# Performance work log

Measured on AMD Instinct MI355X. Metric: run time of the kernel, lower is better.

Reference implementation:

```python
import jax, jax.numpy as jnp
import numpy as np

SYNCNET_T = 5
EMB_D = 512


def _l2norm(x, eps=1e-12):
    return x / jnp.maximum(jnp.linalg.norm(x, axis=-1, keepdims=True), eps)


def setup_inputs() -> dict:
    key = jax.random.key(0)
    k = jax.random.split(key, 6)
    b = 256
    a_1 = jax.random.normal(k[0], (b, 1, 80, 16), dtype=jnp.float32)
    a_2 = jax.random.normal(k[1], (b, 1, 80, 16), dtype=jnp.float32)
    v_1 = jax.random.normal(k[2], (b, 3, SYNCNET_T, 96, 96), dtype=jnp.float32)
    v_2 = jax.random.normal(k[3], (b, 3, SYNCNET_T, 96, 96), dtype=jnp.float32)
    da = 1 * 80 * 16
    dv = 3 * SYNCNET_T * 48 * 96
    W_a = jax.random.normal(k[4], (da, EMB_D), dtype=jnp.float32) / np.float32(np.sqrt(da))
    W_v = jax.random.normal(k[5], (dv, EMB_D), dtype=jnp.float32) / np.float32(np.sqrt(dv))
    return {"a_1": a_1, "v_1": v_1, "a_2": a_2, "v_2": v_2, "W_a": W_a, "W_v": W_v}


def reference(a_1, v_1, a_2, v_2, W_a, W_v):
    b = a_1.shape[0]
    audio = jnp.concatenate([a_1, a_2], axis=0)      # (2b,1,80,16)
    visual = jnp.concatenate([v_1, v_2], axis=0)     # (2b,3,T,96,96)
    visual = visual[:, :, :, visual.shape[3] // 2:]  # lower half -> (2b,3,T,48,96)
    # torch.cat([visual[:,:,i] for i in range(T)], dim=1) -> channel order (T,3)
    n2 = visual.shape[0]
    visual = jnp.moveaxis(visual, 2, 1).reshape(n2, 3 * SYNCNET_T, 48, 96)
    # syncnet (modeled): flatten -> linear -> L2 normalize, 512-d embeddings
    a = _l2norm(audio.reshape(n2, -1) @ W_a)  # (2b,d)
    v = _l2norm(visual.reshape(n2, -1) @ W_v)  # (2b,d)
    a1, a2 = a[:b], a[b:]
    v1, v2 = v[:b], v[b:]
    dot = lambda x, y: jnp.sum(x * y, axis=-1)
    # numerator: product of {a1,a2}x{v1,v2} + combos within audio and within visual
    numerator = (jnp.exp(dot(a1, v1)) + jnp.exp(dot(a1, v2))
                 + jnp.exp(dot(a2, v1)) + jnp.exp(dot(a2, v2))
                 + jnp.exp(dot(a1, a2)) + jnp.exp(dot(v1, v2)))  # (b,)
    # denominator: product of {a1,a2} with ALL visual embeddings v (2b)
    denominator = (jnp.exp(a1 @ v.T) + jnp.exp(a2 @ v.T)).sum(axis=1)  # (b,)
    loss = -jnp.mean(jnp.log(numerator / denominator))
    return loss
```

## Files before the change

### kernel.cpp

```cpp
#include <hip/hip_runtime.h>

typedef __attribute__((ext_vector_type(8))) short bf16x8;
typedef __attribute__((ext_vector_type(4))) float f32x4;

#define KSPLIT_V 16
#define KSPLIT_A 4

__device__ __forceinline__ unsigned int pk2(float a, float b) {
    unsigned int r;
    asm("v_cvt_pk_bf16_f32 %0, %1, %2" : "=v"(r) : "v"(a), "v"(b));
    return r;
}

template<int MODE>
__global__ __launch_bounds__(256, 4) void mm_kernel(
    const float* __restrict__ s1, const float* __restrict__ s2,
    const float* __restrict__ Bsrc, float* __restrict__ outp,
    float* __restrict__ den, float* __restrict__ num)
{
    __shared__ uint4 As[2][256];
    __shared__ uint4 Bs[2][256];

    const int tid = threadIdx.x;
    const int blk = blockIdx.x;

    int m0, n0, k0, nsteps, z = 0;
    if (MODE == 0) {
        const int lin = (blk & 7) * 128 + (blk >> 3);
        z  = lin >> 6;
        m0 = ((lin >> 3) & 7) * 64;
        n0 = (lin & 7) * 64;
        k0 = z * 4320;
        nsteps = 135;
    } else if (MODE == 1) {
        z  = blk >> 6;
        m0 = ((blk >> 3) & 7) * 64;
        n0 = (blk & 7) * 64;
        k0 = z * 320;
        nsteps = 10;
    } else {
        m0 = (blk >> 3) * 64;
        n0 = (blk & 7) * 64;
        k0 = 0;
        nsteps = 16;
    }
    if (MODE != 2) outp += (size_t)z * (512 * 512);

    const int ROWSTR = (MODE == 0) ? 138240 : (MODE == 1 ? 1280 : 512);

    const int a_row = tid >> 2;
    const int a_kb  = tid & 3;
    const int b_col = tid & 63;
    const int b_kb  = tid >> 6;
    const int a_u = (a_kb * 64 + a_row) ^ (a_kb << 1);
    const int b_u = (b_kb * 64 + b_col) ^ (b_kb << 1);

    const int grow = m0 + a_row;
    const float* abase = (grow < 256) ? (s1 + (size_t)grow * ROWSTR)
                                      : (s2 + (size_t)(grow - 256) * ROWSTR);
    int aoff, jj = 0, kglob = k0;
    if (MODE == 0) {
        const int ph = k0 / 4608;
        jj = k0 - ph * 4608;
        const int c = ph % 3, t = ph / 3;
        aoff = c * 46080 + t * 9216 + 4608 + jj + a_kb * 8;
    } else {
        aoff = k0 + a_kb * 8;
    }

    const float* bptr;
    if (MODE == 2) bptr = Bsrc + (size_t)(n0 + b_col) * 512 + b_kb * 8;
    else           bptr = Bsrc + (size_t)(k0 + b_kb * 8) * 512 + n0 + b_col;

    const int lane = tid & 63;
    const int wid  = tid >> 6;
    const int wrow = (wid >> 1) * 32;
    const int wcol = (wid & 1) * 32;
    const int l15  = lane & 15;
    const int lk   = lane >> 4;

    int ra[2], rb[2];
    #pragma unroll
    for (int m = 0; m < 2; ++m) ra[m] = (lk * 64 + wrow + m * 16 + l15) ^ (lk << 1);
    #pragma unroll
    for (int n = 0; n < 2; ++n) rb[n] = (lk * 64 + wcol + n * 16 + l15) ^ (lk << 1);

    f32x4 acc[2][2];
    #pragma unroll
    for (int m = 0; m < 2; ++m)
        #pragma unroll
        for (int n = 0; n < 2; ++n) acc[m][n] = f32x4{0.f, 0.f, 0.f, 0.f};

    float4 A0 = *(const float4*)(abase + aoff);
    float4 A1 = *(const float4*)(abase + aoff + 4);
    float4 B0, B1; float bsr[8];
    if (MODE == 2) {
        B0 = *(const float4*)bptr; B1 = *(const float4*)(bptr + 4);
    } else {
        #pragma unroll
        for (int j = 0; j < 8; ++j) bsr[j] = bptr[(size_t)j * 512];
    }

    for (int ks = 0; ks < nsteps; ++ks) {
        const int cur = ks & 1;

        const bool more = (ks + 1 < nsteps);
        float4 A0n, A1n, B0n, B1n; float bsn[8];
        if (more) {
            kglob += 32;
            if (MODE == 0) {
                aoff += 32; jj += 32;
                if (jj == 4608) {
                    jj = 0;
                    const int ph = kglob / 4608;
                    const int c = ph % 3, t = ph / 3;
                    aoff = c * 46080 + t * 9216 + 4608 + a_kb * 8;
                }
            } else {
                aoff += 32;
            }
            A0n = *(const float4*)(abase + aoff);
            A1n = *(const float4*)(abase + aoff + 4);
            if (MODE == 2) {
                bptr += 32;
                B0n = *(const float4*)bptr; B1n = *(const float4*)(bptr + 4);
            } else {
                bptr += 32 * 512;
                #pragma unroll
                for (int j = 0; j < 8; ++j) bsn[j] = bptr[(size_t)j * 512];
            }
        }

        uint4 pa;
        pa.x = pk2(A0.x, A0.y); pa.y = pk2(A0.z, A0.w);
        pa.z = pk2(A1.x, A1.y); pa.w = pk2(A1.z, A1.w);
        As[cur][a_u] = pa;
        uint4 pb;
        if (MODE == 2) {
            pb.x = pk2(B0.x, B0.y); pb.y = pk2(B0.z, B0.w);
            pb.z = pk2(B1.x, B1.y); pb.w = pk2(B1.z, B1.w);
        } else {
            pb.x = pk2(bsr[0], bsr[1]); pb.y = pk2(bsr[2], bsr[3]);
            pb.z = pk2(bsr[4], bsr[5]); pb.w = pk2(bsr[6], bsr[7]);
        }
        Bs[cur][b_u] = pb;
        __syncthreads();

        bf16x8 af[2], bfr[2];
        #pragma unroll
        for (int m = 0; m < 2; ++m) af[m] = __builtin_bit_cast(bf16x8, As[cur][ra[m]]);
        #pragma unroll
        for (int n = 0; n < 2; ++n) bfr[n] = __builtin_bit_cast(bf16x8, Bs[cur][rb[n]]);
        #pragma unroll
        for (int m = 0; m < 2; ++m)
            #pragma unroll
            for (int n = 0; n < 2; ++n)
                acc[m][n] = __builtin_amdgcn_mfma_f32_16x16x32_bf16(af[m], bfr[n], acc[m][n], 0, 0, 0);

        if (more) {
            A0 = A0n; A1 = A1n;
            if (MODE == 2) { B0 = B0n; B1 = B1n; }
            else {
                #pragma unroll
                for (int j = 0; j < 8; ++j) bsr[j] = bsn[j];
            }
        }
    }

    if (MODE != 2) {
        #pragma unroll
        for (int m = 0; m < 2; ++m)
            #pragma unroll
            for (int n = 0; n < 2; ++n) {
                const int col = n0 + wcol + n * 16 + l15;
                #pragma unroll
                for (int r = 0; r < 4; ++r) {
                    const int row = m0 + wrow + m * 16 + lk * 4 + r;
                    outp[(size_t)row * 512 + col] = acc[m][n][r];
                }
            }
    } else {
        #pragma unroll
        for (int m = 0; m < 2; ++m) {
            float rs[4] = {0.f, 0.f, 0.f, 0.f};
            #pragma unroll
            for (int n = 0; n < 2; ++n) {
                const int col = n0 + wcol + n * 16 + l15;
                #pragma unroll
                for (int r = 0; r < 4; ++r) {
                    const int row = m0 + wrow + m * 16 + lk * 4 + r;
                    const float e = __expf(acc[m][n][r]);
                    rs[r] += e;
                    if (((row - col) & 255) == 0) atomicAdd(num + (row & 255), e);
                }
            }
            #pragma unroll
            for (int r = 0; r < 4; ++r) {
                float v = rs[r];
                v += __shfl_xor(v, 1);
                v += __shfl_xor(v, 2);
                v += __shfl_xor(v, 4);
                v += __shfl_xor(v, 8);
                if (l15 == 0) {
                    const int row = m0 + wrow + m * 16 + lk * 4 + r;
                    atomicAdd(den + (row & 255), v);
                }
            }
        }
    }
}

__global__ __launch_bounds__(256) void norm_kernel(
    const float* __restrict__ partA, const float* __restrict__ partV,
    float* __restrict__ Aout, float* __restrict__ Vout)
{
    const int row = blockIdx.x;
    const int tid = threadIdx.x;
    const bool isV = row >= 512;
    const int r = isV ? (row - 512) : row;
    const int c0 = tid, c1 = tid + 256;

    float v0 = 0.f, v1 = 0.f;
    if (isV) {
        #pragma unroll
        for (int zz = 0; zz < KSPLIT_V; ++zz) {
            const float* p = partV + (size_t)zz * 262144 + (size_t)r * 512;
            v0 += p[c0]; v1 += p[c1];
        }
    } else {
        #pragma unroll
        for (int zz = 0; zz < KSPLIT_A; ++zz) {
            const float* p = partA + (size_t)zz * 262144 + (size_t)r * 512;
            v0 += p[c0]; v1 += p[c1];
        }
    }

    float ss = v0 * v0 + v1 * v1;
    #pragma unroll
    for (int off = 32; off > 0; off >>= 1) ss += __shfl_down(ss, off);
    __shared__ float sbuf[4];
    if ((tid & 63) == 0) sbuf[tid >> 6] = ss;
    __syncthreads();
    const float total = sbuf[0] + sbuf[1] + sbuf[2] + sbuf[3];
    const float inv = 1.f / fmaxf(sqrtf(total), 1e-12f);

    float* outp = (isV ? Vout : Aout) + (size_t)r * 512;
    outp[c0] = v0 * inv;
    outp[c1] = v1 * inv;
}

__global__ __launch_bounds__(512) void zero_kernel(float* __restrict__ p) {
    p[threadIdx.x] = 0.f;
}

__global__ __launch_bounds__(256) void dots_kernel(
    const float* __restrict__ A, const float* __restrict__ V,
    float* __restrict__ num)
{
    const int b = blockIdx.x;
    const int i = b & 255;
    const float* X = (b < 256) ? A : V;
    const float* x = X + (size_t)i * 512;
    const float* y = X + (size_t)(i + 256) * 512;
    const int tid = threadIdx.x;
    float d = x[tid] * y[tid] + x[tid + 256] * y[tid + 256];
    #pragma unroll
    for (int off = 32; off > 0; off >>= 1) d += __shfl_down(d, off);
    __shared__ float sbuf[4];
    if ((tid & 63) == 0) sbuf[tid >> 6] = d;
    __syncthreads();
    if (tid == 0) atomicAdd(num + i, __expf(sbuf[0] + sbuf[1] + sbuf[2] + sbuf[3]));
}

__global__ __launch_bounds__(256) void final_kernel(
    const float* __restrict__ den, const float* __restrict__ num,
    float* __restrict__ out)
{
    const int tid = threadIdx.x;
    float v = logf(den[tid]) - logf(num[tid]);
    #pragma unroll
    for (int off = 32; off > 0; off >>= 1) v += __shfl_down(v, off);
    __shared__ float sbuf[4];
    if ((tid & 63) == 0) sbuf[tid >> 6] = v;
    __syncthreads();
    if (tid == 0) out[0] = (sbuf[0] + sbuf[1] + sbuf[2] + sbuf[3]) * (1.f / 256.f);
}

extern "C" void kernel_launch(void* const* d_in, const int* in_sizes, int n_in,
                              void* d_out, int out_size, void* d_ws, size_t ws_size,
                              hipStream_t stream)
{
    (void)in_sizes; (void)n_in; (void)out_size; (void)ws_size;
    const float* a_1 = (const float*)d_in[0];
    const float* v_1 = (const float*)d_in[1];
    const float* a_2 = (const float*)d_in[2];
    const float* v_2 = (const float*)d_in[3];
    const float* W_a = (const float*)d_in[4];
    const float* W_v = (const float*)d_in[5];
    float* out = (float*)d_out;

    float* ws      = (float*)d_ws;
    float* partV   = ws;
    float* partA   = partV + (size_t)KSPLIT_V * 262144;
    float* Anorm   = partA + (size_t)KSPLIT_A * 262144;
    float* Vnorm   = Anorm + 262144;
    float* den     = Vnorm + 262144;
    float* num     = den + 256;

    zero_kernel<<<1, 512, 0, stream>>>(den);
    mm_kernel<0><<<1024, 256, 0, stream>>>(v_1, v_2, W_v, partV, nullptr, nullptr);
    mm_kernel<1><<<256, 256, 0, stream>>>(a_1, a_2, W_a, partA, nullptr, nullptr);
    norm_kernel<<<1024, 256, 0, stream>>>(partA, partV, Anorm, Vnorm);
    mm_kernel<2><<<64, 256, 0, stream>>>(Anorm, Anorm + 256 * 512, Vnorm, nullptr, den, num);
    dots_kernel<<<512, 256, 0, stream>>>(Anorm, Vnorm, num);
    final_kernel<<<1, 256, 0, stream>>>(den, num, out);
}
```

Measured before the change: 176.0 us.

## Pre-convert inputs and weights to bf16 transposed, use 128x128 direct-to-LDS GEMM

Adds a fused pre-pass that converts W_v and W_a to transposed bf16 and, if the workspace is large enough, also converts the visual and audio activations to contiguous bf16. The main GEMM becomes a 128x128-tile kernel that fills LDS with global_load_lds, with a split-K count chosen from the workspace size. The similarity GEMM moves into its own kernel. The aim is to halve GEMM operand traffic and replace the strided scalar weight loads with wide loads, at the cost of an extra full conversion pass over the 70MB weight every call.

Result: slower. 199.8 us (+13.5%).

```diff
diff --git a/kernel.cpp b/kernel.cpp
--- a/kernel.cpp
+++ b/kernel.cpp
@@ -2,9 +2,6 @@
 
 typedef __attribute__((ext_vector_type(8))) short bf16x8;
 typedef __attribute__((ext_vector_type(4))) float f32x4;
-
-#define KSPLIT_V 16
-#define KSPLIT_A 4
 
 __device__ __forceinline__ unsigned int pk2(float a, float b) {
     unsigned int r;
@@ -12,207 +9,214 @@
     return r;
 }
 
-template<int MODE>
-__global__ __launch_bounds__(256, 4) void mm_kernel(
+__device__ __forceinline__ void gll16(void* lds, const void* g) {
+    __builtin_amdgcn_global_load_lds(
+        (__attribute__((address_space(1))) void*)(uintptr_t)g,
+        (__attribute__((address_space(3))) void*)(uint32_t)(uintptr_t)lds,
+        16, 0, 0);
+}
+
+__global__ __launch_bounds__(256) void conv_fused(
+    const float* __restrict__ v_1, const float* __restrict__ v_2,
+    const float* __restrict__ a_1, const float* __restrict__ a_2,
+    const float* __restrict__ W_v, const float* __restrict__ W_a,
+    unsigned short* __restrict__ Av, unsigned short* __restrict__ Wt,
+    unsigned short* __restrict__ Aa, unsigned short* __restrict__ Wat,
+    int doAv)
+{
+    __shared__ float T[64][65];
+    const int tid = threadIdx.x;
+    const int b = blockIdx.x;
+
+    if (b < 8800) {
+        const float* src; unsigned short* dst; int K, kt, nt;
+        if (b < 8640) { src = W_v; dst = Wt;  K = 69120; kt = b >> 3; nt = b & 7; }
+        else          { src = W_a; dst = Wat; K = 1280;  kt = (b - 8640) >> 3; nt = (b - 8640) & 7; }
+        const int k0 = kt * 64, n0 = nt * 64;
+        #pragma unroll
+        for (int i = 0; i < 4; ++i) {
+            const int kr = i * 16 + (tid >> 4);
+            const int c4 = tid & 15;
+            const float4 f = *(const float4*)(src + (size_t)(k0 + kr) * 512 + n0 + c4 * 4);
+            T[c4 * 4 + 0][kr] = f.x; T[c4 * 4 + 1][kr] = f.y;
+            T[c4 * 4 + 2][kr] = f.z; T[c4 * 4 + 3][kr] = f.w;
+        }
+        __syncthreads();
+        #pragma unroll
+        for (int j = 0; j < 2; ++j) {
+            const int id = j * 256 + tid;
+            const int nl = id >> 3, u = id & 7;
+            float v[8];
+            #pragma unroll
+            for (int kk = 0; kk < 8; ++kk) v[kk] = T[nl][u * 8 + kk];
+            uint4 o;
+            o.x = pk2(v[0], v[1]); o.y = pk2(v[2], v[3]);
+            o.z = pk2(v[4], v[5]); o.w = pk2(v[6], v[7]);
+            *(uint4*)(dst + (size_t)(n0 + nl) * K + k0 + u * 8) = o;
+        }
+    } else if (b < 16480) {
+        if (!doAv) return;
+        const int bb = b - 8800;
+        const int r = bb / 15, p = bb - r * 15;
+        const float* srcb = (r < 256) ? (v_1 + (size_t)r * 138240)
+                                      : (v_2 + (size_t)(r - 256) * 138240);
+        const int c = p % 3, t9 = p / 3;
+        const float* src = srcb + c * 46080 + t9 * 9216 + 4608;
+        unsigned short* dst = Av + (size_t)r * 69120 + p * 4608;
+        #pragma unroll
+        for (int it = 0; it < 5; ++it) {
+            const int u = it * 256 + tid;
+            if (u < 1152) {
+                const float4 f = *(const float4*)(src + u * 4);
+                uint2 o; o.x = pk2(f.x, f.y); o.y = pk2(f.z, f.w);
+                *(uint2*)(dst + u * 4) = o;
+            }
+        }
+    } else {
+        const int idx4 = (b - 16480) * 256 + tid;
+        const int row = idx4 / 320;
+        const int col4 = idx4 - row * 320;
+        const float* src = (row < 256) ? (a_1 + (size_t)row * 1280)
+                                       : (a_2 + (size_t)(row - 256) * 1280);
+        const float4 f = *(const float4*)(src + col4 * 4);
+        uint2 o; o.x = pk2(f.x, f.y); o.y = pk2(f.z, f.w);
+        *(uint2*)(Aa + (size_t)idx4 * 4) = o;
+    }
+}
+
+template<int AMODE>
+__global__ __launch_bounds__(256, 3) void gemm_kernel(
+    const unsigned short* __restrict__ Abf,
     const float* __restrict__ s1, const float* __restrict__ s2,
-    const float* __restrict__ Bsrc, float* __restrict__ outp,
-    float* __restrict__ den, float* __restrict__ num)
-{
-    __shared__ uint4 As[2][256];
-    __shared__ uint4 Bs[2][256];
+    const unsigned short* __restrict__ Bt,
+    float* __restrict__ part, int K, int ksteps)
+{
+    __shared__ uint4 As[1024];
+    __shared__ uint4 Bs[1024];
 
     const int tid = threadIdx.x;
     const int blk = blockIdx.x;
-
-    int m0, n0, k0, nsteps, z = 0;
-    if (MODE == 0) {
-        const int lin = (blk & 7) * 128 + (blk >> 3);
-        z  = lin >> 6;
-        m0 = ((lin >> 3) & 7) * 64;
-        n0 = (lin & 7) * 64;
-        k0 = z * 4320;
-        nsteps = 135;
-    } else if (MODE == 1) {
-        z  = blk >> 6;
-        m0 = ((blk >> 3) & 7) * 64;
-        n0 = (blk & 7) * 64;
-        k0 = z * 320;
-        nsteps = 10;
-    } else {
-        m0 = (blk >> 3) * 64;
-        n0 = (blk & 7) * 64;
-        k0 = 0;
-        nsteps = 16;
-    }
-    if (MODE != 2) outp += (size_t)z * (512 * 512);
-
-    const int ROWSTR = (MODE == 0) ? 138240 : (MODE == 1 ? 1280 : 512);
-
-    const int a_row = tid >> 2;
-    const int a_kb  = tid & 3;
-    const int b_col = tid & 63;
-    const int b_kb  = tid >> 6;
-    const int a_u = (a_kb * 64 + a_row) ^ (a_kb << 1);
-    const int b_u = (b_kb * 64 + b_col) ^ (b_kb << 1);
-
-    const int grow = m0 + a_row;
-    const float* abase = (grow < 256) ? (s1 + (size_t)grow * ROWSTR)
-                                      : (s2 + (size_t)(grow - 256) * ROWSTR);
-    int aoff, jj = 0, kglob = k0;
-    if (MODE == 0) {
-        const int ph = k0 / 4608;
-        jj = k0 - ph * 4608;
-        const int c = ph % 3, t = ph / 3;
-        aoff = c * 46080 + t * 9216 + 4608 + jj + a_kb * 8;
-    } else {
-        aoff = k0 + a_kb * 8;
-    }
-
-    const float* bptr;
-    if (MODE == 2) bptr = Bsrc + (size_t)(n0 + b_col) * 512 + b_kb * 8;
-    else           bptr = Bsrc + (size_t)(k0 + b_kb * 8) * 512 + n0 + b_col;
-
-    const int lane = tid & 63;
-    const int wid  = tid >> 6;
-    const int wrow = (wid >> 1) * 32;
-    const int wcol = (wid & 1) * 32;
-    const int l15  = lane & 15;
-    const int lk   = lane >> 4;
-
-    int ra[2], rb[2];
-    #pragma unroll
-    for (int m = 0; m < 2; ++m) ra[m] = (lk * 64 + wrow + m * 16 + l15) ^ (lk << 1);
-    #pragma unroll
-    for (int n = 0; n < 2; ++n) rb[n] = (lk * 64 + wcol + n * 16 + l15) ^ (lk << 1);
-
-    f32x4 acc[2][2];
-    #pragma unroll
-    for (int m = 0; m < 2; ++m)
-        #pragma unroll
-        for (int n = 0; n < 2; ++n) acc[m][n] = f32x4{0.f, 0.f, 0.f, 0.f};
-
-    float4 A0 = *(const float4*)(abase + aoff);
-    float4 A1 = *(const float4*)(abase + aoff + 4);
-    float4 B0, B1; float bsr[8];
-    if (MODE == 2) {
-        B0 = *(const float4*)bptr; B1 = *(const float4*)(bptr + 4);
-    } else {
-        #pragma unroll
-        for (int j = 0; j < 8; ++j) bsr[j] = bptr[(size_t)j * 512];
-    }
-
-    for (int ks = 0; ks < nsteps; ++ks) {
-        const int cur = ks & 1;
-
-        const bool more = (ks + 1 < nsteps);
-        float4 A0n, A1n, B0n, B1n; float bsn[8];
-        if (more) {
-            kglob += 32;
-            if (MODE == 0) {
-                aoff += 32; jj += 32;
-                if (jj == 4608) {
-                    jj = 0;
-                    const int ph = kglob / 4608;
-                    const int c = ph % 3, t = ph / 3;
-                    aoff = c * 46080 + t * 9216 + 4608 + a_kb * 8;
-                }
-            } else {
-                aoff += 32;
+    const int nwg = gridDim.x;
+    const int cpx = nwg >> 3;
+    const int lin = (blk & 7) * cpx + (blk >> 3);
+    const int z  = lin >> 4;
+    const int mn = lin & 15;
+    const int m0 = (mn >> 2) * 128;
+    const int n0 = (mn & 3) * 128;
+    const int k0 = z * ksteps * 64;
+    part += (size_t)z * 262144;
+
+    const int wid = tid >> 6, lane = tid & 63;
+    const int l15 = lane & 15, lk = lane >> 4;
+    const int wm = (wid >> 1) * 64, wn = (wid & 1) * 64;
+
+    int ua[2][4], ub[2][4];
+    #pragma unroll
+    for (int kh = 0; kh < 2; ++kh) {
+        #pragma unroll
+        for (int mi = 0; mi < 4; ++mi) {
+            const int row = wm + mi * 16 + l15;
+            ua[kh][mi] = row * 8 + ((kh * 4 + lk) ^ (row & 7));
+        }
+        #pragma unroll
+        for (int ni = 0; ni < 4; ++ni) {
+            const int nn = wn + ni * 16 + l15;
+            ub[kh][ni] = nn * 8 + ((kh * 4 + lk) ^ (nn & 7));
+        }
+    }
+
+    const unsigned short* bsrc[4];
+    const unsigned short* asrc[4];
+    #pragma unroll
+    for (int i = 0; i < 4; ++i) {
+        const int u = i * 256 + tid;
+        const int rw = u >> 3, c = u & 7;
+        bsrc[i] = Bt + (size_t)(n0 + rw) * K + k0 + ((c ^ (rw & 7)) * 8);
+        if (AMODE == 0)
+            asrc[i] = Abf + (size_t)(m0 + rw) * K + k0 + ((c ^ (rw & 7)) * 8);
+    }
+    const int a_row = tid >> 1;
+    const float* abase = nullptr;
+    if (AMODE == 1) {
+        const int grow = m0 + a_row;
+        abase = (grow < 256) ? (s1 + (size_t)grow * 138240)
+                             : (s2 + (size_t)(grow - 256) * 138240);
+    }
+
+    f32x4 acc[4][4];
+    #pragma unroll
+    for (int mi = 0; mi < 4; ++mi)
+        #pragma unroll
+        for (int ni = 0; ni < 4; ++ni) acc[mi][ni] = f32x4{0.f, 0.f, 0.f, 0.f};
+
+    int kc = k0;
+    for (int ks = 0; ks < ksteps; ++ks) {
+        #pragma unroll
+        for (int i = 0; i < 4; ++i)
+            gll16(Bs + i * 256 + wid * 64, bsrc[i]);
+        if (AMODE == 0) {
+            #pragma unroll
+            for (int i = 0; i < 4; ++i)
+                gll16(As + i * 256 + wid * 64, asrc[i]);
+        } else {
+            #pragma unroll
+            for (int x4 = 0; x4 < 4; ++x4) {
+                const int x = (tid & 1) * 4 + x4;
+                const int kg = kc + x * 8;
+                const int p = kg / 4608;
+                const int j = kg - p * 4608;
+                const int c3 = p % 3, t9 = p / 3;
+                const float* ap = abase + c3 * 46080 + t9 * 9216 + 4608 + j;
+                const float4 f0 = *(const float4*)ap;
+                const float4 f1 = *(const float4*)(ap + 4);
+                uint4 pa;
+                pa.x = pk2(f0.x, f0.y); pa.y = pk2(f0.z, f0.w);
+                pa.z = pk2(f1.x, f1.y); pa.w = pk2(f1.z, f1.w);
+                As[a_row * 8 + (x ^ (a_row & 7))] = pa;
             }
-            A0n = *(const float4*)(abase + aoff);
-            A1n = *(const float4*)(abase + aoff + 4);
-            if (MODE == 2) {
-                bptr += 32;
-                B0n = *(const float4*)bptr; B1n = *(const float4*)(bptr + 4);
-            } else {
-                bptr += 32 * 512;
+        }
+        __syncthreads();
+
+        #pragma unroll
+        for (int kh = 0; kh < 2; ++kh) {
+            bf16x8 af[4], bfr[4];
+            #pragma unroll
+            for (int mi = 0; mi < 4; ++mi) af[mi] = __builtin_bit_cast(bf16x8, As[ua[kh][mi]]);
+            #pragma unroll
+            for (int ni = 0; ni < 4; ++ni) bfr[ni] = __builtin_bit_cast(bf16x8, Bs[ub[kh][ni]]);
+            #pragma unroll
+            for (int mi = 0; mi < 4; ++mi)
                 #pragma unroll
-                for (int j = 0; j < 8; ++j) bsn[j] = bptr[(size_t)j * 512];
+                for (int ni = 0; ni < 4; ++ni)
+                    acc[mi][ni] = __builtin_amdgcn_mfma_f32_16x16x32_bf16(af[mi], bfr[ni], acc[mi][ni], 0, 0, 0);
+        }
+        __syncthreads();
+
+        kc += 64;
+        #pragma unroll
+        for (int i = 0; i < 4; ++i) bsrc[i] += 64;
+        if (AMODE == 0) {
+            #pragma unroll
+            for (int i = 0; i < 4; ++i) asrc[i] += 64;
+        }
+    }
+
+    #pragma unroll
+    for (int mi = 0; mi < 4; ++mi)
+        #pragma unroll
+        for (int ni = 0; ni < 4; ++ni) {
+            const int col = n0 + wn + ni * 16 + l15;
+            #pragma unroll
+            for (int r = 0; r < 4; ++r) {
+                const int row = m0 + wm + mi * 16 + lk * 4 + r;
+                part[(size_t)row * 512 + col] = acc[mi][ni][r];
             }
         }
-
-        uint4 pa;
-        pa.x = pk2(A0.x, A0.y); pa.y = pk2(A0.z, A0.w);
-        pa.z = pk2(A1.x, A1.y); pa.w = pk2(A1.z, A1.w);
-        As[cur][a_u] = pa;
-        uint4 pb;
-        if (MODE == 2) {
-            pb.x = pk2(B0.x, B0.y); pb.y = pk2(B0.z, B0.w);
-            pb.z = pk2(B1.x, B1.y); pb.w = pk2(B1.z, B1.w);
-        } else {
-            pb.x = pk2(bsr[0], bsr[1]); pb.y = pk2(bsr[2], bsr[3]);
-            pb.z = pk2(bsr[4], bsr[5]); pb.w = pk2(bsr[6], bsr[7]);
-        }
-        Bs[cur][b_u] = pb;
-        __syncthreads();
-
-        bf16x8 af[2], bfr[2];
-        #pragma unroll
-        for (int m = 0; m < 2; ++m) af[m] = __builtin_bit_cast(bf16x8, As[cur][ra[m]]);
-        #pragma unroll
-        for (int n = 0; n < 2; ++n) bfr[n] = __builtin_bit_cast(bf16x8, Bs[cur][rb[n]]);
-        #pragma unroll
-        for (int m = 0; m < 2; ++m)
-            #pragma unroll
-            for (int n = 0; n < 2; ++n)
-                acc[m][n] = __builtin_amdgcn_mfma_f32_16x16x32_bf16(af[m], bfr[n], acc[m][n], 0, 0, 0);
-
-        if (more) {
-            A0 = A0n; A1 = A1n;
-            if (MODE == 2) { B0 = B0n; B1 = B1n; }
-            else {
-                #pragma unroll
-                for (int j = 0; j < 8; ++j) bsr[j] = bsn[j];
-            }
-        }
-    }
-
-    if (MODE != 2) {
-        #pragma unroll
-        for (int m = 0; m < 2; ++m)
-            #pragma unroll
-            for (int n = 0; n < 2; ++n) {
-                const int col = n0 + wcol + n * 16 + l15;
-                #pragma unroll
-                for (int r = 0; r < 4; ++r) {
-                    const int row = m0 + wrow + m * 16 + lk * 4 + r;
-                    outp[(size_t)row * 512 + col] = acc[m][n][r];
-                }
-            }
-    } else {
-        #pragma unroll
-        for (int m = 0; m < 2; ++m) {
-            float rs[4] = {0.f, 0.f, 0.f, 0.f};
-            #pragma unroll
-            for (int n = 0; n < 2; ++n) {
-                const int col = n0 + wcol + n * 16 + l15;
-                #pragma unroll
-                for (int r = 0; r < 4; ++r) {
-                    const int row = m0 + wrow + m * 16 + lk * 4 + r;
-                    const float e = __expf(acc[m][n][r]);
-                    rs[r] += e;
-                    if (((row - col) & 255) == 0) atomicAdd(num + (row & 255), e);
-                }
-            }
-            #pragma unroll
-            for (int r = 0; r < 4; ++r) {
-                float v = rs[r];
-                v += __shfl_xor(v, 1);
-                v += __shfl_xor(v, 2);
-                v += __shfl_xor(v, 4);
-                v += __shfl_xor(v, 8);
-                if (l15 == 0) {
-                    const int row = m0 + wrow + m * 16 + lk * 4 + r;
-                    atomicAdd(den + (row & 255), v);
-                }
-            }
-        }
-    }
 }
 
 __global__ __launch_bounds__(256) void norm_kernel(
     const float* __restrict__ partA, const float* __restrict__ partV,
-    float* __restrict__ Aout, float* __restrict__ Vout)
+    float* __restrict__ Aout, float* __restrict__ Vout, int nzV)
 {
     const int row = blockIdx.x;
     const int tid = threadIdx.x;
@@ -222,14 +226,13 @@
 
     float v0 = 0.f, v1 = 0.f;
     if (isV) {
-        #pragma unroll
-        for (int zz = 0; zz < KSPLIT_V; ++zz) {
+        for (int zz = 0; zz < nzV; ++zz) {
             const float* p = partV + (size_t)zz * 262144 + (size_t)r * 512;
             v0 += p[c0]; v1 += p[c1];
         }
     } else {
         #pragma unroll
-        for (int zz = 0; zz < KSPLIT_A; ++zz) {
+        for (int zz = 0; zz < 2; ++zz) {
             const float* p = partA + (size_t)zz * 262144 + (size_t)r * 512;
             v0 += p[c0]; v1 += p[c1];
         }
@@ -249,6 +252,112 @@
     outp[c1] = v1 * inv;
 }
 
+__global__ __launch_bounds__(256) void sim_kernel(
+    const float* __restrict__ A, const float* __restrict__ V,
+    float* __restrict__ den, float* __restrict__ num)
+{
+    __shared__ uint4 As[2][256];
+    __shared__ uint4 Bs[2][256];
+
+    const int tid = threadIdx.x;
+    const int m0 = (blockIdx.x >> 3) * 64;
+    const int n0 = (blockIdx.x & 7) * 64;
+    const int nsteps = 16;
+
+    const int a_row = tid >> 2, a_kb = tid & 3;
+    const int b_col = tid & 63, b_kb = tid >> 6;
+    const int a_u = (a_kb * 64 + a_row) ^ (a_kb << 1);
+    const int b_u = (b_kb * 64 + b_col) ^ (b_kb << 1);
+
+    const float* abase = A + (size_t)(m0 + a_row) * 512;
+    const float* bptr  = V + (size_t)(n0 + b_col) * 512 + b_kb * 8;
+    int aoff = a_kb * 8;
+
+    const int lane = tid & 63, wid = tid >> 6;
+    const int wrow = (wid >> 1) * 32, wcol = (wid & 1) * 32;
+    const int l15 = lane & 15, lk = lane >> 4;
+
+    int ra[2], rb[2];
+    #pragma unroll
+    for (int m = 0; m < 2; ++m) ra[m] = (lk * 64 + wrow + m * 16 + l15) ^ (lk << 1);
+    #pragma unroll
+    for (int n = 0; n < 2; ++n) rb[n] = (lk * 64 + wcol + n * 16 + l15) ^ (lk << 1);
+
+    f32x4 acc[2][2];
+    #pragma unroll
+    for (int m = 0; m < 2; ++m)
+        #pragma unroll
+        for (int n = 0; n < 2; ++n) acc[m][n] = f32x4{0.f, 0.f, 0.f, 0.f};
+
+    float4 A0 = *(const float4*)(abase + aoff);
+    float4 A1 = *(const float4*)(abase + aoff + 4);
+    float4 B0 = *(const float4*)bptr;
+    float4 B1 = *(const float4*)(bptr + 4);
+
+    for (int ks = 0; ks < nsteps; ++ks) {
+        const int cur = ks & 1;
+        const bool more = (ks + 1 < nsteps);
+        float4 A0n, A1n, B0n, B1n;
+        if (more) {
+            aoff += 32; bptr += 32;
+            A0n = *(const float4*)(abase + aoff);
+            A1n = *(const float4*)(abase + aoff + 4);
+            B0n = *(const float4*)bptr;
+            B1n = *(const float4*)(bptr + 4);
+        }
+        uint4 pa;
+        pa.x = pk2(A0.x, A0.y); pa.y = pk2(A0.z, A0.w);
+        pa.z = pk2(A1.x, A1.y); pa.w = pk2(A1.z, A1.w);
+        As[cur][a_u] = pa;
+        uint4 pb;
+        pb.x = pk2(B0.x, B0.y); pb.y = pk2(B0.z, B0.w);
+        pb.z = pk2(B1.x, B1.y); pb.w = pk2(B1.z, B1.w);
+        Bs[cur][b_u] = pb;
+        __syncthreads();
+
+        bf16x8 af[2], bfr[2];
+        #pragma unroll
+        for (int m = 0; m < 2; ++m) af[m] = __builtin_bit_cast(bf16x8, As[cur][ra[m]]);
+        #pragma unroll
+        for (int n = 0; n < 2; ++n) bfr[n] = __builtin_bit_cast(bf16x8, Bs[cur][rb[n]]);
+        #pragma unroll
+        for (int m = 0; m < 2; ++m)
+            #pragma unroll
+            for (int n = 0; n < 2; ++n)
+                acc[m][n] = __builtin_amdgcn_mfma_f32_16x16x32_bf16(af[m], bfr[n], acc[m][n], 0, 0, 0);
+
+        if (more) { A0 = A0n; A1 = A1n; B0 = B0n; B1 = B1n; }
+    }
+
+    #pragma unroll
+    for (int m = 0; m < 2; ++m) {
+        float rs[4] = {0.f, 0.f, 0.f, 0.f};
+        #pragma unroll
+        for (int n = 0; n < 2; ++n) {
+            const int col = n0 + wcol + n * 16 + l15;
+            #pragma unroll
+            for (int r = 0; r < 4; ++r) {
+                const int row = m0 + wrow + m * 16 + lk * 4 + r;
+                const float e = __expf(acc[m][n][r]);
+                rs[r] += e;
+                if (((row - col) & 255) == 0) atomicAdd(num + (row & 255), e);
+            }
+        }
+        #pragma unroll
+        for (int r = 0; r < 4; ++r) {
+            float v = rs[r];
+            v += __shfl_xor(v, 1);
+            v += __shfl_xor(v, 2);
+            v += __shfl_xor(v, 4);
+            v += __shfl_xor(v, 8);
+            if (l15 == 0) {
+                const int row = m0 + wrow + m * 16 + lk * 4 + r;
+                atomicAdd(den + (row & 255), v);
+            }
+        }
+    }
+}
+
 __global__ __launch_bounds__(512) void zero_kernel(float* __restrict__ p) {
     p[threadIdx.x] = 0.f;
 }
@@ -290,7 +399,7 @@
                               void* d_out, int out_size, void* d_ws, size_t ws_size,
                               hipStream_t stream)
 {
-    (void)in_sizes; (void)n_in; (void)out_size; (void)ws_size;
+    (void)in_sizes; (void)n_in; (void)out_size;
     const float* a_1 = (const float*)d_in[0];
     const float* v_1 = (const float*)d_in[1];
     const float* a_2 = (const float*)d_in[2];
@@ -299,19 +408,47 @@
     const float* W_v = (const float*)d_in[5];
     float* out = (float*)d_out;
 
-    float* ws      = (float*)d_ws;
-    float* partV   = ws;
-    float* partA   = partV + (size_t)KSPLIT_V * 262144;
-    float* Anorm   = partA + (size_t)KSPLIT_A * 262144;
-    float* Vnorm   = Anorm + 262144;
-    float* den     = Vnorm + 262144;
-    float* num     = den + 256;
+    const size_t F_BASE = 512  + 2 * 262144  + 2 * 262144
+                        + 2 * 327680  + 17694720 ;
+    auto bytes_for = [&](int kv, bool av) {
+        return (F_BASE + (size_t)kv * 262144 + (av ? 17694720u : 0u)) * 4;
+    };
+    int KV; bool AV;
+    if      (ws_size >= bytes_for(45, true))  { KV = 45; AV = true;  }
+    else if (ws_size >= bytes_for(45, false)) { KV = 45; AV = false; }
+    else if (ws_size >= bytes_for(15, false)) { KV = 15; AV = false; }
+    else                                      { KV = 8;  AV = false; }
+    const int kstepsV = 1080 / KV;
+
+    float* cur = (float*)d_ws;
+    float* den   = cur; cur += 256;
+    float* num   = cur; cur += 256;
+    float* Anorm = cur; cur += 262144;
+    float* Vnorm = cur; cur += 262144;
+    float* partA = cur; cur += 2 * 262144;
+    unsigned short* Aa  = (unsigned short*)cur; cur += 327680;
+    unsigned short* Wat = (unsigned short*)cur; cur += 327680;
+    float* partV = cur; cur += (size_t)KV * 262144;
+    unsigned short* Wt = (unsigned short*)cur; cur += 17694720;
+    unsigned short* Av = (unsigned short*)cur;
 
     zero_kernel<<<1, 512, 0, stream>>>(den);
-    mm_kernel<0><<<1024, 256, 0, stream>>>(v_1, v_2, W_v, partV, nullptr, nullptr);
-    mm_kernel<1><<<256, 256, 0, stream>>>(a_1, a_2, W_a, partA, nullptr, nullptr);
-    norm_kernel<<<1024, 256, 0, stream>>>(partA, partV, Anorm, Vnorm);
-    mm_kernel<2><<<64, 256, 0, stream>>>(Anorm, Anorm + 256 * 512, Vnorm, nullptr, den, num);
+
+    conv_fused<<<17120, 256, 0, stream>>>(v_1, v_2, a_1, a_2, W_v, W_a,
+                                          Av, Wt, Aa, Wat, AV ? 1 : 0);
+
+    if (AV)
+        gemm_kernel<0><<<16 * KV, 256, 0, stream>>>(Av, nullptr, nullptr, Wt,
+                                                    partV, 69120, kstepsV);
+    else
+        gemm_kernel<1><<<16 * KV, 256, 0, stream>>>(nullptr, v_1, v_2, Wt,
+                                                    partV, 69120, kstepsV);
+
+    gemm_kernel<0><<<32, 256, 0, stream>>>(Aa, nullptr, nullptr, Wat,
+                                           partA, 1280, 10);
+
+    norm_kernel<<<1024, 256, 0, stream>>>(partA, partV, Anorm, Vnorm, KV);
+    sim_kernel<<<64, 256, 0, stream>>>(Anorm, Vnorm, den, num);
     dots_kernel<<<512, 256, 0, stream>>>(Anorm, Vnorm, num);
     final_kernel<<<1, 256, 0, stream>>>(den, num, out);
 }
```
